# Optimization experiments

Measured on AMD Instinct MI355X. Metric: run time of the kernel, lower is better.

The kernel has to match this reference:

```python
import jax, jax.numpy as jnp
import numpy as np

B, L, N, H = 512, 50, 16, 128
NUM_USERS = NUM_ITEMS = 100000


def setup_inputs() -> dict:
    key = jax.random.key(0)
    ks = jax.random.split(key, 20)
    s = lambda i, shape: jax.random.normal(ks[i], shape, dtype=jnp.float32) * 0.05
    return {
        "user_ids": jax.random.randint(ks[0], (B,), 0, NUM_USERS),
        "item_ids": jax.random.randint(ks[1], (B,), 0, NUM_ITEMS),
        "history": jax.random.randint(ks[2], (B, L), 0, NUM_ITEMS),
        "neighbor_emb": jax.random.normal(ks[3], (B, L, N, H), dtype=jnp.float32),
        "user_table": s(4, (NUM_USERS, H)),
        "item_table": s(5, (NUM_ITEMS, H)),
        "Wa": s(6, (2 * H, 96)), "ba": jnp.zeros((96,), jnp.float32),
        "W1": s(7, (96, 48)), "b1": jnp.zeros((48,), jnp.float32),
        "W2": s(8, (48, 16)), "b2": jnp.zeros((16,), jnp.float32),
        "W3": s(9, (16, 1)), "b3": jnp.zeros((1,), jnp.float32),
        # 4 heads of Linear(H, H//4) concatenated on the output dim == one [H, H] GEMM
        "Wmh": s(10, (H, H)), "bmh": jnp.zeros((H,), jnp.float32),
        "Wfc1": s(11, (2 * H, H)), "bfc1": jnp.zeros((H,), jnp.float32),
        "Wout": s(12, (H, 1)), "bout": jnp.zeros((1,), jnp.float32),
    }


def reference(user_ids, item_ids, history, neighbor_emb,
              user_table, item_table, Wa, ba, W1, b1, W2, b2, W3, b3,
              Wmh, bmh, Wfc1, bfc1, Wout, bout):
    user_emb = user_table[user_ids]                      # [B, H]
    item_emb = item_table[item_ids]                      # computed but unused (as in original)
    hist_emb = item_table[history]                       # [B, L, H]

    # concat(history broadcast over neighbors, neighbor_emb) -> [B, L, N, 2H]
    hist_b = jnp.broadcast_to(hist_emb[:, :, None, :], (B, L, N, H))
    att_in = jnp.concatenate([hist_b, neighbor_emb], axis=-1)

    scores = jax.nn.relu(att_in @ Wa + ba)               # [B, L, N, 96]
    h1 = jax.nn.relu(scores @ W1 + b1)                   # [B, L, N, 48]
    h2 = jax.nn.relu(h1 @ W2 + b2)                       # [B, L, N, 16]
    logits = (h2 @ W3 + b3)[..., 0]                      # [B, L, N]
    attn = jax.nn.softmax(logits, axis=-1)               # softmax over neighbor dim

    agg = jnp.einsum('bln,blnh->blh', attn, neighbor_emb)  # [B, L, H]
    mh = agg @ Wmh + bmh                                 # fused multihead projections
    pooled = mh.mean(axis=1)                             # [B, H]

    comb = jnp.concatenate([user_emb, pooled], axis=-1)  # [B, 2H]
    hidden = jax.nn.relu(comb @ Wfc1 + bfc1)             # dropout is identity in eval
    out = jax.nn.sigmoid(hidden @ Wout + bout)[:, 0]     # [B]
    return out
```

## Files before the change

### kernel.cpp

```cpp
#include <hip/hip_runtime.h>

constexpr int B  = 512, L = 50, N = 16, H = 128;
constexpr int C1 = 96, C2 = 48, C3 = 16;

typedef __bf16   bf16x8 __attribute__((ext_vector_type(8)));
typedef float    f32x4  __attribute__((ext_vector_type(4)));
typedef unsigned u32x4  __attribute__((ext_vector_type(4)));

__device__ __forceinline__ bf16x8 cvt8(float4 a, float4 b) {
  bf16x8 r;
  r[0] = (__bf16)a.x; r[1] = (__bf16)a.y; r[2] = (__bf16)a.z; r[3] = (__bf16)a.w;
  r[4] = (__bf16)b.x; r[5] = (__bf16)b.y; r[6] = (__bf16)b.z; r[7] = (__bf16)b.w;
  return r;
}
__device__ __forceinline__ float bf16lo(unsigned u) { return __uint_as_float(u << 16); }
__device__ __forceinline__ float bf16hi(unsigned u) { return __uint_as_float(u & 0xffff0000u); }
__device__ __forceinline__ unsigned pkbf(float lo, float hi) {
  unsigned r;
  asm("v_cvt_pk_bf16_f32 %0, %1, %2" : "=v"(r) : "v"(lo), "v"(hi));
  return r;
}

__global__ __launch_bounds__(512, 1) void fused_kernel(
    const int*   __restrict__ user_ids,
    const int*   __restrict__ history,
    const float* __restrict__ neighbor_emb,
    const float* __restrict__ user_table,
    const float* __restrict__ item_table,
    const float* __restrict__ Wa,  const float* __restrict__ ba,
    const float* __restrict__ W1,  const float* __restrict__ b1,
    const float* __restrict__ W2,  const float* __restrict__ b2,
    const float* __restrict__ W3,
    const float* __restrict__ Wmh,  const float* __restrict__ bmh,
    const float* __restrict__ Wfc1, const float* __restrict__ bfc1,
    const float* __restrict__ Wout, const float* __restrict__ bout,
    float* __restrict__ out)
{
  __shared__ __align__(16) __bf16 sWa[48 * 64 * 8];
  __shared__ __align__(16) __bf16 sW1[9 * 64 * 8];
  __shared__ __align__(16) __bf16 sHS[8][16 * C1];
  __shared__ float sRed[8][128];
  __shared__ float sAgg2[2][128];
  __shared__ float sComb[2][2 * H];
  __shared__ float sP[8];

  const int tid  = threadIdx.x;
  const int wave = tid >> 6;
  const int lane = tid & 63;
  const int g    = lane >> 4;
  const int c    = lane & 15;

  for (int e = tid; e < 48 * 64; e += 512) {
    int lv = e & 63, frag = e >> 6;
    int s = frag & 7, t = frag >> 3;
    int k0 = s * 32 + ((lv >> 4) << 3);
    int cc = t * 16 + (lv & 15);
    bf16x8 v;
    #pragma unroll
    for (int j = 0; j < 8; ++j) v[j] = (__bf16)Wa[(k0 + j) * C1 + cc];
    *(bf16x8*)&sWa[e * 8] = v;
  }
  for (int e = tid; e < 9 * 64; e += 512) {
    int lv = e & 63, frag = e >> 6;
    int s = frag % 3, t = frag / 3;
    int k0 = s * 32 + ((lv >> 4) << 3);
    int cc = t * 16 + (lv & 15);
    bf16x8 v;
    #pragma unroll
    for (int j = 0; j < 8; ++j) v[j] = (__bf16)W1[(k0 + j) * C2 + cc];
    *(bf16x8*)&sW1[e * 8] = v;
  }

  const f32x4 b1v0 = *(const f32x4*)&b1[ 0 + 4 * g];
  const f32x4 b1v1 = *(const f32x4*)&b1[16 + 4 * g];
  const f32x4 b1v2 = *(const f32x4*)&b1[32 + 4 * g];
  const f32x4 b2v  = *(const f32x4*)&b2[4 * g];
  const f32x4 w3v  = *(const f32x4*)&W3[4 * g];
  bf16x8 w2f[2];
  #pragma unroll
  for (int s = 0; s < 2; ++s)
    #pragma unroll
    for (int j = 0; j < 8; ++j) {
      int k = s * 32 + g * 8 + j;
      w2f[s][j] = (k < C2) ? (__bf16)W2[k * C3 + c] : (__bf16)0.f;
    }

  __syncthreads();

  const int bb = blockIdx.x * 2 + (wave >> 2);
  const int wl = wave & 3;
  __bf16* HS = sHS[wave];
  const int nIter = (L - wl + 3) / 4;

  {
    float ba_r[6];
    #pragma unroll
    for (int t = 0; t < 6; ++t) ba_r[t] = ba[t * 16 + c];
    int li  = wl + 4 * c;
    int idx = (li < L) ? history[bb * L + li] : history[bb * L];
    const float* hr = item_table + (size_t)idx * H;
    f32x4 acch[6];
    #pragma unroll
    for (int t = 0; t < 6; ++t) acch[t] = (f32x4){0.f, 0.f, 0.f, 0.f};
    #pragma unroll
    for (int s = 0; s < 4; ++s) {
      const float* p = hr + s * 32 + g * 8;
      bf16x8 a = cvt8(*(const float4*)p, *(const float4*)(p + 4));
      #pragma unroll
      for (int t = 0; t < 6; ++t)
        acch[t] = __builtin_amdgcn_mfma_f32_16x16x32_bf16(
            a, *(const bf16x8*)&sWa[((t * 8 + s) * 64 + lane) * 8], acch[t], 0, 0, 0);
    }
    #pragma unroll
    for (int t = 0; t < 6; ++t)
      #pragma unroll
      for (int r = 0; r < 4; ++r)
        HS[(4 * g + r) * C1 + t * 16 + c] = (__bf16)(acch[t][r] + ba_r[t]);
  }

  const float* nb0 = neighbor_emb + (size_t)(bb * L + wl) * (N * H) + c * H + g * 8;
  float4 nf[8];
  {
    const float* p = nb0;
    #pragma unroll
    for (int s = 0; s < 4; ++s) {
      nf[2 * s]     = *(const float4*)(p + s * 32);
      nf[2 * s + 1] = *(const float4*)(p + s * 32 + 4);
    }
  }
  float aggp[32];
  #pragma unroll
  for (int i = 0; i < 32; ++i) aggp[i] = 0.f;

  const int  src_lo = ((g & 1) << 5) | c;
  const int  src_hi = src_lo + 16;
  const bool gh     = (g >> 1) & 1;

  for (int it = 0; it < nIter; ++it) {
    bf16x8 aA[4];
    #pragma unroll
    for (int s = 0; s < 4; ++s) aA[s] = cvt8(nf[2 * s], nf[2 * s + 1]);
    if (it + 1 < nIter) {
      const float* p = nb0 + (size_t)(it + 1) * (4 * N * H);
      #pragma unroll
      for (int s = 0; s < 4; ++s) {
        nf[2 * s]     = *(const float4*)(p + s * 32);
        nf[2 * s + 1] = *(const float4*)(p + s * 32 + 4);
      }
    }

    f32x4 acc[6];
    #pragma unroll
    for (int t = 0; t < 6; ++t) {
      uint2 hw = *(const uint2*)&HS[it * C1 + 16 * t + 4 * g];
      acc[t][0] = bf16lo(hw.x); acc[t][1] = bf16hi(hw.x);
      acc[t][2] = bf16lo(hw.y); acc[t][3] = bf16hi(hw.y);
    }
    #pragma unroll
    for (int s = 0; s < 4; ++s)
      #pragma unroll
      for (int t = 0; t < 6; ++t)
        acc[t] = __builtin_amdgcn_mfma_f32_16x16x32_bf16(
            *(const bf16x8*)&sWa[((t * 8 + 4 + s) * 64 + lane) * 8], aA[s],
            acc[t], 0, 0, 0);
    unsigned pku[6][2];
    #pragma unroll
    for (int t = 0; t < 6; ++t) {
      pku[t][0] = pkbf(fmaxf(acc[t][0], 0.f), fmaxf(acc[t][1], 0.f));
      pku[t][1] = pkbf(fmaxf(acc[t][2], 0.f), fmaxf(acc[t][3], 0.f));
    }

    f32x4 acc2[3] = {b1v0, b1v1, b1v2};
    #pragma unroll
    for (int s = 0; s < 3; ++s) {
      unsigned a0 = __shfl((int)pku[2 * s][0], src_lo);
      unsigned a1 = __shfl((int)pku[2 * s][1], src_lo);
      unsigned a2 = __shfl((int)pku[2 * s][0], src_hi);
      unsigned a3 = __shfl((int)pku[2 * s][1], src_hi);
      unsigned d0 = __shfl((int)pku[2 * s + 1][0], src_lo);
      unsigned d1 = __shfl((int)pku[2 * s + 1][1], src_lo);
      unsigned d2 = __shfl((int)pku[2 * s + 1][0], src_hi);
      unsigned d3 = __shfl((int)pku[2 * s + 1][1], src_hi);
      u32x4 wv = {gh ? d0 : a0, gh ? d1 : a1, gh ? d2 : a2, gh ? d3 : a3};
      bf16x8 bf2 = __builtin_bit_cast(bf16x8, wv);
      #pragma unroll
      for (int t2 = 0; t2 < 3; ++t2)
        acc2[t2] = __builtin_amdgcn_mfma_f32_16x16x32_bf16(
            *(const bf16x8*)&sW1[((t2 * 3 + s) * 64 + lane) * 8], bf2,
            acc2[t2], 0, 0, 0);
    }
    unsigned pk2[3][2];
    #pragma unroll
    for (int t2 = 0; t2 < 3; ++t2) {
      pk2[t2][0] = pkbf(fmaxf(acc2[t2][0], 0.f), fmaxf(acc2[t2][1], 0.f));
      pk2[t2][1] = pkbf(fmaxf(acc2[t2][2], 0.f), fmaxf(acc2[t2][3], 0.f));
    }

    f32x4 acc3 = b2v;
    {
      unsigned a0 = __shfl((int)pk2[0][0], src_lo);
      unsigned a1 = __shfl((int)pk2[0][1], src_lo);
      unsigned a2 = __shfl((int)pk2[0][0], src_hi);
      unsigned a3 = __shfl((int)pk2[0][1], src_hi);
      unsigned d0 = __shfl((int)pk2[1][0], src_lo);
      unsigned d1 = __shfl((int)pk2[1][1], src_lo);
      unsigned d2 = __shfl((int)pk2[1][0], src_hi);
      unsigned d3 = __shfl((int)pk2[1][1], src_hi);
      u32x4 wv = {gh ? d0 : a0, gh ? d1 : a1, gh ? d2 : a2, gh ? d3 : a3};
      acc3 = __builtin_amdgcn_mfma_f32_16x16x32_bf16(
          w2f[0], __builtin_bit_cast(bf16x8, wv), acc3, 0, 0, 0);
      unsigned e0 = __shfl((int)pk2[2][0], src_lo);
      unsigned e1 = __shfl((int)pk2[2][1], src_lo);
      unsigned e2 = __shfl((int)pk2[2][0], src_hi);
      unsigned e3 = __shfl((int)pk2[2][1], src_hi);
      u32x4 wv2 = {gh ? 0u : e0, gh ? 0u : e1, gh ? 0u : e2, gh ? 0u : e3};
      acc3 = __builtin_amdgcn_mfma_f32_16x16x32_bf16(
          w2f[1], __builtin_bit_cast(bf16x8, wv2), acc3, 0, 0, 0);
    }

    float lg = 0.f;
    #pragma unroll
    for (int r = 0; r < 4; ++r) lg = fmaf(fmaxf(acc3[r], 0.f), w3v[r], lg);
    lg += __shfl_xor(lg, 16);
    lg += __shfl_xor(lg, 32);
    float e = __expf(lg);
    float se = e;
    se += __shfl_xor(se, 1);
    se += __shfl_xor(se, 2);
    se += __shfl_xor(se, 4);
    se += __shfl_xor(se, 8);
    const float w = e / se;

    #pragma unroll
    for (int s = 0; s < 4; ++s) {
      u32x4 au = __builtin_bit_cast(u32x4, aA[s]);
      #pragma unroll
      for (int q = 0; q < 4; ++q) {
        unsigned u = au[q];
        aggp[s * 8 + 2 * q]     = fmaf(w, bf16lo(u), aggp[s * 8 + 2 * q]);
        aggp[s * 8 + 2 * q + 1] = fmaf(w, bf16hi(u), aggp[s * 8 + 2 * q + 1]);
      }
    }
  }

  #pragma unroll
  for (int off = 1; off < 16; off <<= 1)
    #pragma unroll
    for (int i = 0; i < 32; ++i) aggp[i] += __shfl_xor(aggp[i], off);
  if (c == 0) {
    #pragma unroll
    for (int s = 0; s < 4; ++s) {
      float4 v0 = {aggp[8 * s + 0], aggp[8 * s + 1], aggp[8 * s + 2], aggp[8 * s + 3]};
      float4 v1 = {aggp[8 * s + 4], aggp[8 * s + 5], aggp[8 * s + 6], aggp[8 * s + 7]};
      *(float4*)&sRed[wave][32 * s + 8 * g]     = v0;
      *(float4*)&sRed[wave][32 * s + 8 * g + 4] = v1;
    }
  }
  __syncthreads();

  const int bs  = tid >> 8;
  const int t2  = tid & 255;
  const int bb2 = blockIdx.x * 2 + bs;
  if (t2 < 128) {
    float s = 0.f;
    #pragma unroll
    for (int w = 0; w < 4; ++w) s += sRed[bs * 4 + w][t2];
    sAgg2[bs][t2] = s * (1.0f / L);
    sComb[bs][t2] = user_table[(size_t)user_ids[bb2] * H + t2];
  }
  __syncthreads();
  if (t2 < 128) {
    float p = bmh[t2];
    #pragma unroll 8
    for (int k = 0; k < H; ++k) p = fmaf(sAgg2[bs][k], Wmh[k * H + t2], p);
    sComb[bs][H + t2] = p;
  }
  __syncthreads();
  float partial = 0.f;
  if (t2 < 128) {
    float hd = bfc1[t2];
    #pragma unroll 8
    for (int k = 0; k < 2 * H; ++k) hd = fmaf(sComb[bs][k], Wfc1[k * H + t2], hd);
    hd = fmaxf(hd, 0.f);
    partial = hd * Wout[t2];
  }
  #pragma unroll
  for (int off = 32; off > 0; off >>= 1) partial += __shfl_down(partial, off);
  if (lane == 0) sP[wave] = partial;
  __syncthreads();
  if (tid < 2) {
    float s = sP[tid * 4] + sP[tid * 4 + 1] + bout[0];
    out[blockIdx.x * 2 + tid] = 1.f / (1.f + __expf(-s));
  }
}

extern "C" void kernel_launch(void* const* d_in, const int* in_sizes, int n_in,
                              void* d_out, int out_size, void* d_ws, size_t ws_size,
                              hipStream_t stream) {
  const int*   user_ids     = (const int*)  d_in[0];
  const int*   history      = (const int*)  d_in[2];
  const float* neighbor_emb = (const float*)d_in[3];
  const float* user_table   = (const float*)d_in[4];
  const float* item_table   = (const float*)d_in[5];
  const float* Wa   = (const float*)d_in[6];
  const float* ba   = (const float*)d_in[7];
  const float* W1   = (const float*)d_in[8];
  const float* b1   = (const float*)d_in[9];
  const float* W2   = (const float*)d_in[10];
  const float* b2   = (const float*)d_in[11];
  const float* W3   = (const float*)d_in[12];
  const float* Wmh  = (const float*)d_in[14];
  const float* bmh  = (const float*)d_in[15];
  const float* Wfc1 = (const float*)d_in[16];
  const float* bfc1 = (const float*)d_in[17];
  const float* Wout = (const float*)d_in[18];
  const float* bout = (const float*)d_in[19];

  float* out = (float*)d_out;

  hipLaunchKernelGGL(fused_kernel, dim3(B / 2), dim3(512), 0, stream,
                     user_ids, history, neighbor_emb, user_table, item_table,
                     Wa, ba, W1, b1, W2, b2, W3,
                     Wmh, bmh, Wfc1, bfc1, Wout, bout, out);
}
```

Baseline: 64.83 us.

## Process two neighbor rows per iteration and keep aggregation accumulators in packed bf16

The attention-weight MLP chain is factored into a helper and the main loop now handles two l-rows per iteration. This gives two independent MFMA/shuffle dependency chains to interleave, and the next two rows' neighbor loads are prefetched with double buffering. The weighted-sum accumulator is packed into 16 bf16 registers instead of 32 floats to offset the extra register pressure. Rounding the running sum to bf16 after every step loses accuracy over up to 13 steps.

After: 84.04 us. +29.6%, slower.

```diff
diff --git a/kernel.cpp b/kernel.cpp
--- a/kernel.cpp
+++ b/kernel.cpp
@@ -19,6 +19,96 @@
   unsigned r;
   asm("v_cvt_pk_bf16_f32 %0, %1, %2" : "=v"(r) : "v"(lo), "v"(hi));
   return r;
+}
+
+__device__ __forceinline__ float attn_weight(
+    const bf16x8 (&aA)[4], const __bf16* __restrict__ HSrow,
+    const __bf16* __restrict__ sWa, const __bf16* __restrict__ sW1,
+    const bf16x8 (&w2f)[2],
+    f32x4 b1v0, f32x4 b1v1, f32x4 b1v2, f32x4 b2v, f32x4 w3v,
+    int lane, int g, int src_lo, int src_hi, bool gh)
+{
+  f32x4 acc[6];
+  #pragma unroll
+  for (int t = 0; t < 6; ++t) {
+    uint2 hw = *(const uint2*)&HSrow[16 * t + 4 * g];
+    acc[t][0] = bf16lo(hw.x); acc[t][1] = bf16hi(hw.x);
+    acc[t][2] = bf16lo(hw.y); acc[t][3] = bf16hi(hw.y);
+  }
+  #pragma unroll
+  for (int s = 0; s < 4; ++s)
+    #pragma unroll
+    for (int t = 0; t < 6; ++t)
+      acc[t] = __builtin_amdgcn_mfma_f32_16x16x32_bf16(
+          *(const bf16x8*)&sWa[((t * 8 + 4 + s) * 64 + lane) * 8], aA[s],
+          acc[t], 0, 0, 0);
+  unsigned pku[6][2];
+  #pragma unroll
+  for (int t = 0; t < 6; ++t) {
+    pku[t][0] = pkbf(fmaxf(acc[t][0], 0.f), fmaxf(acc[t][1], 0.f));
+    pku[t][1] = pkbf(fmaxf(acc[t][2], 0.f), fmaxf(acc[t][3], 0.f));
+  }
+
+  f32x4 acc2[3] = {b1v0, b1v1, b1v2};
+  #pragma unroll
+  for (int s = 0; s < 3; ++s) {
+    unsigned a0 = __shfl((int)pku[2 * s][0], src_lo);
+    unsigned a1 = __shfl((int)pku[2 * s][1], src_lo);
+    unsigned a2 = __shfl((int)pku[2 * s][0], src_hi);
+    unsigned a3 = __shfl((int)pku[2 * s][1], src_hi);
+    unsigned d0 = __shfl((int)pku[2 * s + 1][0], src_lo);
+    unsigned d1 = __shfl((int)pku[2 * s + 1][1], src_lo);
+    unsigned d2 = __shfl((int)pku[2 * s + 1][0], src_hi);
+    unsigned d3 = __shfl((int)pku[2 * s + 1][1], src_hi);
+    u32x4 wv = {gh ? d0 : a0, gh ? d1 : a1, gh ? d2 : a2, gh ? d3 : a3};
+    bf16x8 bf2 = __builtin_bit_cast(bf16x8, wv);
+    #pragma unroll
+    for (int t2 = 0; t2 < 3; ++t2)
+      acc2[t2] = __builtin_amdgcn_mfma_f32_16x16x32_bf16(
+          *(const bf16x8*)&sW1[((t2 * 3 + s) * 64 + lane) * 8], bf2,
+          acc2[t2], 0, 0, 0);
+  }
+  unsigned pk2[3][2];
+  #pragma unroll
+  for (int t2 = 0; t2 < 3; ++t2) {
+    pk2[t2][0] = pkbf(fmaxf(acc2[t2][0], 0.f), fmaxf(acc2[t2][1], 0.f));
+    pk2[t2][1] = pkbf(fmaxf(acc2[t2][2], 0.f), fmaxf(acc2[t2][3], 0.f));
+  }
+
+  f32x4 acc3 = b2v;
+  {
+    unsigned a0 = __shfl((int)pk2[0][0], src_lo);
+    unsigned a1 = __shfl((int)pk2[0][1], src_lo);
+    unsigned a2 = __shfl((int)pk2[0][0], src_hi);
+    unsigned a3 = __shfl((int)pk2[0][1], src_hi);
+    unsigned d0 = __shfl((int)pk2[1][0], src_lo);
+    unsigned d1 = __shfl((int)pk2[1][1], src_lo);
+    unsigned d2 = __shfl((int)pk2[1][0], src_hi);
+    unsigned d3 = __shfl((int)pk2[1][1], src_hi);
+    u32x4 wv = {gh ? d0 : a0, gh ? d1 : a1, gh ? d2 : a2, gh ? d3 : a3};
+    acc3 = __builtin_amdgcn_mfma_f32_16x16x32_bf16(
+        w2f[0], __builtin_bit_cast(bf16x8, wv), acc3, 0, 0, 0);
+    unsigned e0 = __shfl((int)pk2[2][0], src_lo);
+    unsigned e1 = __shfl((int)pk2[2][1], src_lo);
+    unsigned e2 = __shfl((int)pk2[2][0], src_hi);
+    unsigned e3 = __shfl((int)pk2[2][1], src_hi);
+    u32x4 wv2 = {gh ? 0u : e0, gh ? 0u : e1, gh ? 0u : e2, gh ? 0u : e3};
+    acc3 = __builtin_amdgcn_mfma_f32_16x16x32_bf16(
+        w2f[1], __builtin_bit_cast(bf16x8, wv2), acc3, 0, 0, 0);
+  }
+
+  float lg = 0.f;
+  #pragma unroll
+  for (int r = 0; r < 4; ++r) lg = fmaf(fmaxf(acc3[r], 0.f), w3v[r], lg);
+  lg += __shfl_xor(lg, 16);
+  lg += __shfl_xor(lg, 32);
+  float e = __expf(lg);
+  float se = e;
+  se += __shfl_xor(se, 1);
+  se += __shfl_xor(se, 2);
+  se += __shfl_xor(se, 4);
+  se += __shfl_xor(se, 8);
+  return e / se;
 }
 
 __global__ __launch_bounds__(512, 1) void fused_kernel(
@@ -119,139 +209,111 @@
   }
 
   const float* nb0 = neighbor_emb + (size_t)(bb * L + wl) * (N * H) + c * H + g * 8;
-  float4 nf[8];
+  const size_t TS = (size_t)4 * N * H;
+
+  float4 nfA[8], nfB[8];
   {
-    const float* p = nb0;
-    #pragma unroll
-    for (int s = 0; s < 4; ++s) {
-      nf[2 * s]     = *(const float4*)(p + s * 32);
-      nf[2 * s + 1] = *(const float4*)(p + s * 32 + 4);
-    }
-  }
-  float aggp[32];
-  #pragma unroll
-  for (int i = 0; i < 32; ++i) aggp[i] = 0.f;
+    const float* p0 = nb0;
+    const float* p1 = nb0 + TS;
+    #pragma unroll
+    for (int s = 0; s < 4; ++s) {
+      nfA[2 * s]     = *(const float4*)(p0 + s * 32);
+      nfA[2 * s + 1] = *(const float4*)(p0 + s * 32 + 4);
+      nfB[2 * s]     = *(const float4*)(p1 + s * 32);
+      nfB[2 * s + 1] = *(const float4*)(p1 + s * 32 + 4);
+    }
+  }
+  unsigned agp[16];
+  #pragma unroll
+  for (int i = 0; i < 16; ++i) agp[i] = 0u;
 
   const int  src_lo = ((g & 1) << 5) | c;
   const int  src_hi = src_lo + 16;
   const bool gh     = (g >> 1) & 1;
 
-  for (int it = 0; it < nIter; ++it) {
-    bf16x8 aA[4];
-    #pragma unroll
-    for (int s = 0; s < 4; ++s) aA[s] = cvt8(nf[2 * s], nf[2 * s + 1]);
-    if (it + 1 < nIter) {
-      const float* p = nb0 + (size_t)(it + 1) * (4 * N * H);
+  const int nPair = nIter >> 1;
+  for (int pr = 0; pr < nPair; ++pr) {
+    const int it0 = 2 * pr;
+    bf16x8 aA0[4], aA1[4];
+    #pragma unroll
+    for (int s = 0; s < 4; ++s) {
+      aA0[s] = cvt8(nfA[2 * s], nfA[2 * s + 1]);
+      aA1[s] = cvt8(nfB[2 * s], nfB[2 * s + 1]);
+    }
+    if (it0 + 2 < nIter) {
+      const float* p = nb0 + (size_t)(it0 + 2) * TS;
       #pragma unroll
       for (int s = 0; s < 4; ++s) {
-        nf[2 * s]     = *(const float4*)(p + s * 32);
-        nf[2 * s + 1] = *(const float4*)(p + s * 32 + 4);
+        nfA[2 * s]     = *(const float4*)(p + s * 32);
+        nfA[2 * s + 1] = *(const float4*)(p + s * 32 + 4);
       }
     }
-
-    f32x4 acc[6];
-    #pragma unroll
-    for (int t = 0; t < 6; ++t) {
-      uint2 hw = *(const uint2*)&HS[it * C1 + 16 * t + 4 * g];
-      acc[t][0] = bf16lo(hw.x); acc[t][1] = bf16hi(hw.x);
-      acc[t][2] = bf16lo(hw.y); acc[t][3] = bf16hi(hw.y);
-    }
-    #pragma unroll
-    for (int s = 0; s < 4; ++s)
-      #pragma unroll
-      for (int t = 0; t < 6; ++t)
-        acc[t] = __builtin_amdgcn_mfma_f32_16x16x32_bf16(
-            *(const bf16x8*)&sWa[((t * 8 + 4 + s) * 64 + lane) * 8], aA[s],
-            acc[t], 0, 0, 0);
-    unsigned pku[6][2];
-    #pragma unroll
-    for (int t = 0; t < 6; ++t) {
-      pku[t][0] = pkbf(fmaxf(acc[t][0], 0.f), fmaxf(acc[t][1], 0.f));
-      pku[t][1] = pkbf(fmaxf(acc[t][2], 0.f), fmaxf(acc[t][3], 0.f));
-    }
-
-    f32x4 acc2[3] = {b1v0, b1v1, b1v2};
-    #pragma unroll
-    for (int s = 0; s < 3; ++s) {
-      unsigned a0 = __shfl((int)pku[2 * s][0], src_lo);
-      unsigned a1 = __shfl((int)pku[2 * s][1], src_lo);
-      unsigned a2 = __shfl((int)pku[2 * s][0], src_hi);
-      unsigned a3 = __shfl((int)pku[2 * s][1], src_hi);
-      unsigned d0 = __shfl((int)pku[2 * s + 1][0], src_lo);
-      unsigned d1 = __shfl((int)pku[2 * s + 1][1], src_lo);
-      unsigned d2 = __shfl((int)pku[2 * s + 1][0], src_hi);
-      unsigned d3 = __shfl((int)pku[2 * s + 1][1], src_hi);
-      u32x4 wv = {gh ? d0 : a0, gh ? d1 : a1, gh ? d2 : a2, gh ? d3 : a3};
-      bf16x8 bf2 = __builtin_bit_cast(bf16x8, wv);
-      #pragma unroll
-      for (int t2 = 0; t2 < 3; ++t2)
-        acc2[t2] = __builtin_amdgcn_mfma_f32_16x16x32_bf16(
-            *(const bf16x8*)&sW1[((t2 * 3 + s) * 64 + lane) * 8], bf2,
-            acc2[t2], 0, 0, 0);
-    }
-    unsigned pk2[3][2];
-    #pragma unroll
-    for (int t2 = 0; t2 < 3; ++t2) {
-      pk2[t2][0] = pkbf(fmaxf(acc2[t2][0], 0.f), fmaxf(acc2[t2][1], 0.f));
-      pk2[t2][1] = pkbf(fmaxf(acc2[t2][2], 0.f), fmaxf(acc2[t2][3], 0.f));
-    }
-
-    f32x4 acc3 = b2v;
-    {
-      unsigned a0 = __shfl((int)pk2[0][0], src_lo);
-      unsigned a1 = __shfl((int)pk2[0][1], src_lo);
-      unsigned a2 = __shfl((int)pk2[0][0], src_hi);
-      unsigned a3 = __shfl((int)pk2[0][1], src_hi);
-      unsigned d0 = __shfl((int)pk2[1][0], src_lo);
-      unsigned d1 = __shfl((int)pk2[1][1], src_lo);
-      unsigned d2 = __shfl((int)pk2[1][0], src_hi);
-      unsigned d3 = __shfl((int)pk2[1][1], src_hi);
-      u32x4 wv = {gh ? d0 : a0, gh ? d1 : a1, gh ? d2 : a2, gh ? d3 : a3};
-      acc3 = __builtin_amdgcn_mfma_f32_16x16x32_bf16(
-          w2f[0], __builtin_bit_cast(bf16x8, wv), acc3, 0, 0, 0);
-      unsigned e0 = __shfl((int)pk2[2][0], src_lo);
-      unsigned e1 = __shfl((int)pk2[2][1], src_lo);
-      unsigned e2 = __shfl((int)pk2[2][0], src_hi);
-      unsigned e3 = __shfl((int)pk2[2][1], src_hi);
-      u32x4 wv2 = {gh ? 0u : e0, gh ? 0u : e1, gh ? 0u : e2, gh ? 0u : e3};
-      acc3 = __builtin_amdgcn_mfma_f32_16x16x32_bf16(
-          w2f[1], __builtin_bit_cast(bf16x8, wv2), acc3, 0, 0, 0);
-    }
-
-    float lg = 0.f;
-    #pragma unroll
-    for (int r = 0; r < 4; ++r) lg = fmaf(fmaxf(acc3[r], 0.f), w3v[r], lg);
-    lg += __shfl_xor(lg, 16);
-    lg += __shfl_xor(lg, 32);
-    float e = __expf(lg);
-    float se = e;
-    se += __shfl_xor(se, 1);
-    se += __shfl_xor(se, 2);
-    se += __shfl_xor(se, 4);
-    se += __shfl_xor(se, 8);
-    const float w = e / se;
-
-    #pragma unroll
-    for (int s = 0; s < 4; ++s) {
-      u32x4 au = __builtin_bit_cast(u32x4, aA[s]);
+    if (it0 + 3 < nIter) {
+      const float* p = nb0 + (size_t)(it0 + 3) * TS;
+      #pragma unroll
+      for (int s = 0; s < 4; ++s) {
+        nfB[2 * s]     = *(const float4*)(p + s * 32);
+        nfB[2 * s + 1] = *(const float4*)(p + s * 32 + 4);
+      }
+    }
+
+    float w0 = attn_weight(aA0, HS + (size_t)it0 * C1, sWa, sW1, w2f,
+                           b1v0, b1v1, b1v2, b2v, w3v,
+                           lane, g, src_lo, src_hi, gh);
+    float w1 = attn_weight(aA1, HS + (size_t)(it0 + 1) * C1, sWa, sW1, w2f,
+                           b1v0, b1v1, b1v2, b2v, w3v,
+                           lane, g, src_lo, src_hi, gh);
+
+    #pragma unroll
+    for (int s = 0; s < 4; ++s) {
+      u32x4 a0 = __builtin_bit_cast(u32x4, aA0[s]);
+      u32x4 a1 = __builtin_bit_cast(u32x4, aA1[s]);
       #pragma unroll
       for (int q = 0; q < 4; ++q) {
-        unsigned u = au[q];
-        aggp[s * 8 + 2 * q]     = fmaf(w, bf16lo(u), aggp[s * 8 + 2 * q]);
-        aggp[s * 8 + 2 * q + 1] = fmaf(w, bf16hi(u), aggp[s * 8 + 2 * q + 1]);
+        unsigned p = agp[s * 4 + q];
+        float lo = bf16lo(p), hi = bf16hi(p);
+        lo = fmaf(w0, bf16lo(a0[q]), lo);
+        lo = fmaf(w1, bf16lo(a1[q]), lo);
+        hi = fmaf(w0, bf16hi(a0[q]), hi);
+        hi = fmaf(w1, bf16hi(a1[q]), hi);
+        agp[s * 4 + q] = pkbf(lo, hi);
       }
     }
   }
-
+  if (nIter & 1) {
+    bf16x8 aA0[4];
+    #pragma unroll
+    for (int s = 0; s < 4; ++s) aA0[s] = cvt8(nfA[2 * s], nfA[2 * s + 1]);
+    float w0 = attn_weight(aA0, HS + (size_t)(nIter - 1) * C1, sWa, sW1, w2f,
+                           b1v0, b1v1, b1v2, b2v, w3v,
+                           lane, g, src_lo, src_hi, gh);
+    #pragma unroll
+    for (int s = 0; s < 4; ++s) {
+      u32x4 a0 = __builtin_bit_cast(u32x4, aA0[s]);
+      #pragma unroll
+      for (int q = 0; q < 4; ++q) {
+        unsigned p = agp[s * 4 + q];
+        agp[s * 4 + q] = pkbf(fmaf(w0, bf16lo(a0[q]), bf16lo(p)),
+                              fmaf(w0, bf16hi(a0[q]), bf16hi(p)));
+      }
+    }
+  }
+
+  float aggf[32];
+  #pragma unroll
+  for (int i = 0; i < 16; ++i) {
+    aggf[2 * i]     = bf16lo(agp[i]);
+    aggf[2 * i + 1] = bf16hi(agp[i]);
+  }
   #pragma unroll
   for (int off = 1; off < 16; off <<= 1)
     #pragma unroll
-    for (int i = 0; i < 32; ++i) aggp[i] += __shfl_xor(aggp[i], off);
+    for (int i = 0; i < 32; ++i) aggf[i] += __shfl_xor(aggf[i], off);
   if (c == 0) {
     #pragma unroll
     for (int s = 0; s < 4; ++s) {
-      float4 v0 = {aggp[8 * s + 0], aggp[8 * s + 1], aggp[8 * s + 2], aggp[8 * s + 3]};
-      float4 v1 = {aggp[8 * s + 4], aggp[8 * s + 5], aggp[8 * s + 6], aggp[8 * s + 7]};
+      float4 v0 = {aggf[8 * s + 0], aggf[8 * s + 1], aggf[8 * s + 2], aggf[8 * s + 3]};
+      float4 v1 = {aggf[8 * s + 4], aggf[8 * s + 5], aggf[8 * s + 6], aggf[8 * s + 7]};
       *(float4*)&sRed[wave][32 * s + 8 * g]     = v0;
       *(float4*)&sRed[wave][32 * s + 8 * g + 4] = v1;
     }
```
